# Optimization experiments

Hardware: AMD Instinct MI355X
Metric: run time of the kernel (lower is better)

Reference implementation:

```python
import jax, jax.numpy as jnp
import numpy as np

N_NODES = 10000
N_EDGES = 320000
IN_DIM = 256
HID = 64
HEADS = 4
OUT_DIM = 64
NEG_SLOPE = 0.2


def setup_inputs() -> dict:
    key = jax.random.key(0)
    ks = jax.random.split(key, 10)
    s = 0.05
    return {
        "h": jax.random.normal(ks[0], (N_NODES, IN_DIM), jnp.float32),
        "src": jax.random.randint(ks[1], (N_EDGES,), 0, N_NODES, jnp.int32),
        "dst": jax.random.randint(ks[2], (N_EDGES,), 0, N_NODES, jnp.int32),
        "W1": jax.random.normal(ks[3], (IN_DIM, HEADS * HID), jnp.float32) * s,
        "al1": jax.random.normal(ks[4], (HEADS, HID), jnp.float32) * s,
        "ar1": jax.random.normal(ks[5], (HEADS, HID), jnp.float32) * s,
        "b1": jnp.zeros((HEADS * HID,), jnp.float32),
        "W2": jax.random.normal(ks[6], (HEADS * HID, OUT_DIM), jnp.float32) * s,
        "al2": jax.random.normal(ks[7], (1, OUT_DIM), jnp.float32) * s,
        "ar2": jax.random.normal(ks[8], (1, OUT_DIM), jnp.float32) * s,
        "b2": jnp.zeros((OUT_DIM,), jnp.float32),
    }


def _gatconv(h, W, al, ar, b, src, dst, n_heads, d_out):
    """DGL-style GATConv: project, edge-softmax attention, scatter-aggregate."""
    n = h.shape[0]
    feat = (h @ W).reshape(n, n_heads, d_out)          # [N,H,D]
    el = jnp.sum(feat * al, axis=-1)                   # [N,H]
    er = jnp.sum(feat * ar, axis=-1)                   # [N,H]
    e = jax.nn.leaky_relu(el[src] + er[dst], NEG_SLOPE)  # [E,H]
    # segment softmax over incoming edges of each dst node
    m = jax.ops.segment_max(e, dst, num_segments=n)    # [N,H]
    ex = jnp.exp(e - m[dst])                           # [E,H]
    denom = jax.ops.segment_sum(ex, dst, num_segments=n)  # [N,H]
    alpha = ex / denom[dst]                            # [E,H]
    msg = feat[src] * alpha[:, :, None]                # [E,H,D]
    out = jax.ops.segment_sum(msg, dst, num_segments=n)  # [N,H,D]
    return out + b.reshape(n_heads, d_out)


def reference(h, src, dst, W1, al1, ar1, b1, W2, al2, ar2, b2):
    h1 = _gatconv(h, W1, al1, ar1, b1, src, dst, HEADS, HID)
    h1 = jax.nn.elu(h1.reshape(N_NODES, HEADS * HID))  # flatten(1) then ELU
    h2 = _gatconv(h1, W2, al2, ar2, b2, src, dst, 1, OUT_DIM)
    return jnp.squeeze(h2, axis=1)  # [N, OUT_DIM]
```

## Files before the change

kernel.cpp:

```cpp
#include <hip/hip_runtime.h>
#include <hip/hip_bf16.h>
#include <stdint.h>

#define NN 10000
#define NE 320000
#define NH 4
#define BCAP 128

#define GEMM1_MT 157
#define GEMM1_BLOCKS (GEMM1_MT * 4)
#define BUILD_BLOCKS 1250

typedef __attribute__((ext_vector_type(8))) short s16x8;
typedef __attribute__((ext_vector_type(4))) float f32x4;
typedef __attribute__((ext_vector_type(8))) unsigned short u16x8;

static __device__ __forceinline__ float b2f(unsigned short u) {
    union { unsigned int i; float f; } x; x.i = ((unsigned int)u) << 16; return x.f;
}
static __device__ __forceinline__ unsigned short f2b(float f) {
    unsigned int u = __float_as_uint(f);
    unsigned int r = (u + 0x7fffu + ((u >> 16) & 1u)) >> 16;
    return (unsigned short)r;
}

__global__ __launch_bounds__(256) void k_prep(const unsigned short* __restrict__ hraw,
                        const void* __restrict__ W1, const void* __restrict__ W2,
                        const void* al1, const void* ar1, const void* b1,
                        const void* al2, const void* ar2, const void* b2,
                        unsigned short* __restrict__ W1T, unsigned short* __restrict__ W2T,
                        unsigned short* __restrict__ canon, int* __restrict__ cnt,
                        int* __restrict__ flag) {
    __shared__ int sb[256];
    int t = threadIdx.x;
    int c = 0;
    for (int i = t; i < 2048; i += 256) {
        unsigned short u = hraw[i];
        int e = (u >> 7) & 0xFF;
        c += (e >= 97 && e <= 157) ? 1 : 0;
    }
    sb[t] = c;
    __syncthreads();
    for (int o = 128; o > 0; o >>= 1) {
        if (t < o) sb[t] += sb[t + o];
        __syncthreads();
    }
    int isbf = (sb[0] >= 1741) ? 1 : 0;

    int idx = blockIdx.x * 256 + t;
    if (idx < 65536) {
        int n = idx >> 8, k = idx & 255;
        W1T[idx] = isbf ? ((const unsigned short*)W1)[k * 256 + n]
                        : f2b(((const float*)W1)[k * 256 + n]);
    } else if (idx < 81920) {
        int j = idx - 65536;
        int n = j >> 8, k = j & 255;
        W2T[j] = isbf ? ((const unsigned short*)W2)[k * 64 + n]
                      : f2b(((const float*)W2)[k * 64 + n]);
    } else if (idx < 82880) {
        int j = idx - 81920;
        const void* srcp; int q;
        if      (j < 256) { srcp = al1; q = j; }
        else if (j < 512) { srcp = ar1; q = j - 256; }
        else if (j < 768) { srcp = b1;  q = j - 512; }
        else if (j < 832) { srcp = al2; q = j - 768; }
        else if (j < 896) { srcp = ar2; q = j - 832; }
        else              { srcp = b2;  q = j - 896; }
        canon[j] = isbf ? ((const unsigned short*)srcp)[q] : f2b(((const float*)srcp)[q]);
    } else if (idx < 92880) {
        cnt[idx - 82880] = 0;
    } else if (idx == 92880) {
        flag[0] = isbf;
    }
}

#define BSTRIDE 264
static __device__ __forceinline__ void gemm_body(short* Bs,
                        const void* __restrict__ A, const unsigned short* __restrict__ BT,
                        unsigned short* __restrict__ C,
                        float* __restrict__ el, float* __restrict__ er,
                        const unsigned short* __restrict__ al,
                        const unsigned short* __restrict__ ar,
                        int M, int N, int H, int a_isbf, int mtile, int head) {
    int t = threadIdx.x;
    int wave = t >> 6, lane = t & 63;
    int m0 = mtile * 64;
    const unsigned short* Bh = BT + (size_t)head * 64 * 256;

#pragma unroll
    for (int i = 0; i < 8; ++i) {
        int idx = t + i * 256;
        int row = idx >> 5, chunk = idx & 31;
        *(s16x8*)&Bs[row * BSTRIDE + chunk * 8] =
            *(const s16x8*)&Bh[(size_t)row * 256 + chunk * 8];
    }
    __syncthreads();

    int kq = (lane >> 4) * 8;
    const unsigned short* Ab = (const unsigned short*)A;
    const float*          Af = (const float*)A;
    int aRow = m0 + wave * 16 + (lane & 15);
    int aR = (aRow < M) ? aRow : M - 1;
    f32x4 acc[4] = {};

#pragma unroll
    for (int k0 = 0; k0 < 256; k0 += 32) {
        s16x8 afr;
        if (a_isbf) {
            afr = *(const s16x8*)&Ab[(size_t)aR * 256 + k0 + kq];
        } else {
            const float* pf = &Af[(size_t)aR * 256 + k0 + kq];
            float4 x0 = *(const float4*)pf;
            float4 x1 = *(const float4*)(pf + 4);
            afr[0] = (short)f2b(x0.x); afr[1] = (short)f2b(x0.y);
            afr[2] = (short)f2b(x0.z); afr[3] = (short)f2b(x0.w);
            afr[4] = (short)f2b(x1.x); afr[5] = (short)f2b(x1.y);
            afr[6] = (short)f2b(x1.z); afr[7] = (short)f2b(x1.w);
        }
#pragma unroll
        for (int nt = 0; nt < 4; ++nt) {
            s16x8 bfr = *(const s16x8*)&Bs[(nt * 16 + (lane & 15)) * BSTRIDE + k0 + kq];
            acc[nt] = __builtin_amdgcn_mfma_f32_16x16x32_bf16(afr, bfr, acc[nt], 0, 0, 0);
        }
    }

    float alv[4], arv[4];
#pragma unroll
    for (int nt = 0; nt < 4; ++nt) {
        int c = (lane & 15) + nt * 16;
        alv[nt] = b2f(al[head * 64 + c]);
        arv[nt] = b2f(ar[head * 64 + c]);
    }
    int col0 = head * 64 + (lane & 15);
    int r0 = m0 + wave * 16 + (lane >> 4) * 4;
    float cr[4][4];
#pragma unroll
    for (int nt = 0; nt < 4; ++nt) {
        int col = col0 + nt * 16;
#pragma unroll
        for (int i = 0; i < 4; ++i) {
            unsigned short cb = f2b(acc[nt][i]);
            cr[nt][i] = b2f(cb);
            int r = r0 + i;
            if (r < M) C[(size_t)r * N + col] = cb;
        }
    }
#pragma unroll
    for (int i = 0; i < 4; ++i) {
        float pl = 0.f, pr = 0.f;
#pragma unroll
        for (int nt = 0; nt < 4; ++nt) {
            pl += cr[nt][i] * alv[nt];
            pr += cr[nt][i] * arv[nt];
        }
#pragma unroll
        for (int o = 1; o < 16; o <<= 1) {
            pl += __shfl_xor(pl, o, 64);
            pr += __shfl_xor(pr, o, 64);
        }
        int r = r0 + i;
        if ((lane & 15) == 0 && r < M) {
            el[(size_t)r * H + head] = pl;
            er[(size_t)r * H + head] = pr;
        }
    }
}

__global__ __launch_bounds__(256) void k_g1b(const void* __restrict__ A,
                        const unsigned short* __restrict__ W1T,
                        unsigned short* __restrict__ feat1,
                        float* __restrict__ el, float* __restrict__ er,
                        const unsigned short* __restrict__ al,
                        const unsigned short* __restrict__ ar,
                        const int* __restrict__ flagp,
                        const int* __restrict__ src, const int* __restrict__ dst,
                        int* __restrict__ cnt, int* __restrict__ bucket) {
    __shared__ short Bs[64 * BSTRIDE];
    int bid = blockIdx.x;
    if (bid < GEMM1_BLOCKS) {
        int head = bid / GEMM1_MT;
        int mtile = bid - head * GEMM1_MT;
        gemm_body(Bs, A, W1T, feat1, el, er, al, ar, NN, 256, NH, flagp[0], mtile, head);
    } else {
        int i = (bid - GEMM1_BLOCKS) * 256 + threadIdx.x;
        if (i < NE) {
            int d = dst[i];
            int pos = atomicAdd(&cnt[d], 1);
            if (pos < BCAP) bucket[(d << 7) + pos] = src[i];
        }
    }
}

__global__ __launch_bounds__(256, 8) void k_e1h(const int* __restrict__ cnt,
                        const int* __restrict__ bucket,
                        const float* __restrict__ el, const float* __restrict__ er,
                        const unsigned short* __restrict__ feat,
                        const unsigned short* __restrict__ b1,
                        unsigned short* __restrict__ h1) {
    int wave = threadIdx.x >> 6, lane = threadIdx.x & 63;
    int bid = blockIdx.x;
    int head = bid / 2500;
    int node = (bid - head * 2500) * 4 + wave;
    int eg = lane >> 3, d8 = lane & 7;
    int end = cnt[node]; if (end > BCAP) end = BCAP;
    const int* bkt = bucket + ((size_t)node << 7);
    float er_d = er[(size_t)node * 4 + head];

    if (end <= 64) {
        int s = 0; float w = 0.f;
        if (lane < end) {
            s = bkt[lane];
            float x = el[(size_t)s * 4 + head] + er_d;
            x = (x >= 0.f) ? x : 0.2f * x;
            w = __expf(x);
        }
        float ls = w;
#pragma unroll
        for (int o = 1; o < 64; o <<= 1) ls += __shfl_xor(ls, o, 64);
        float a[8] = {};
        int niter = (end + 7) >> 3;
#pragma unroll 4
        for (int i = 0; i < niter; ++i) {
            int idx = 8 * i + eg;
            int   se = __shfl(s, idx, 64);
            float we = __shfl(w, idx, 64);
            u16x8 fv = *(const u16x8*)&feat[(((size_t)se * NH + head) << 6) + (d8 << 3)];
#pragma unroll
            for (int j = 0; j < 8; ++j) a[j] += we * b2f(fv[j]);
        }
#pragma unroll
        for (int j = 0; j < 8; ++j) {
            a[j] += __shfl_xor(a[j], 8, 64);
            a[j] += __shfl_xor(a[j], 16, 64);
            a[j] += __shfl_xor(a[j], 32, 64);
        }
        if (eg == 0) {
            float inv = (ls > 0.f) ? 1.f / ls : 0.f;
            u16x8 r;
#pragma unroll
            for (int j = 0; j < 8; ++j) {
                float o = a[j] * inv + b2f(b1[head * 64 + d8 * 8 + j]);
                o = (o > 0.f) ? o : (__expf(o) - 1.f);
                r[j] = f2b(o);
            }
            *(u16x8*)&h1[(((size_t)node * NH + head) << 6) + d8 * 8] = r;
        }
    } else {
        float a[8] = {};
        float ls = 0.f;
        for (int base = 0; base < end; base += 64) {
            int c = base + lane;
            int s = 0; float w = 0.f;
            if (c < end) {
                s = bkt[c];
                float x = el[(size_t)s * 4 + head] + er_d;
                x = (x >= 0.f) ? x : 0.2f * x;
                w = __expf(x);
            }
            ls += w;
            int cn = end - base; if (cn > 64) cn = 64;
            int niter = (cn + 7) >> 3;
#pragma unroll 2
            for (int i = 0; i < niter; ++i) {
                int idx = 8 * i + eg;
                int   se = __shfl(s, idx, 64);
                float we = __shfl(w, idx, 64);
                u16x8 fv = *(const u16x8*)&feat[(((size_t)se * NH + head) << 6) + (d8 << 3)];
#pragma unroll
                for (int j = 0; j < 8; ++j) a[j] += we * b2f(fv[j]);
            }
        }
#pragma unroll
        for (int o = 1; o < 64; o <<= 1) ls += __shfl_xor(ls, o, 64);
#pragma unroll
        for (int j = 0; j < 8; ++j) {
            a[j] += __shfl_xor(a[j], 8, 64);
            a[j] += __shfl_xor(a[j], 16, 64);
            a[j] += __shfl_xor(a[j], 32, 64);
        }
        if (eg == 0) {
            float inv = (ls > 0.f) ? 1.f / ls : 0.f;
            u16x8 r;
#pragma unroll
            for (int j = 0; j < 8; ++j) {
                float o = a[j] * inv + b2f(b1[head * 64 + d8 * 8 + j]);
                o = (o > 0.f) ? o : (__expf(o) - 1.f);
                r[j] = f2b(o);
            }
            *(u16x8*)&h1[(((size_t)node * NH + head) << 6) + d8 * 8] = r;
        }
    }
}

__global__ __launch_bounds__(256) void k_gemm(const void* __restrict__ A,
                                              const unsigned short* __restrict__ BT,
                                              unsigned short* __restrict__ C,
                                              float* __restrict__ el, float* __restrict__ er,
                                              const unsigned short* __restrict__ al,
                                              const unsigned short* __restrict__ ar,
                                              int M, int N, int H) {
    __shared__ short Bs[64 * BSTRIDE];
    gemm_body(Bs, A, BT, C, el, er, al, ar, M, N, H, 1, blockIdx.x, blockIdx.y);
}

__global__ __launch_bounds__(256, 4) void k_edge2(const int* __restrict__ cnt,
                        const int* __restrict__ bucket,
                        const float* __restrict__ el, const float* __restrict__ er,
                        const unsigned short* __restrict__ feat,
                        const unsigned short* __restrict__ b2,
                        void* __restrict__ out, const int* __restrict__ flagp) {
    int wave = threadIdx.x >> 6, lane = threadIdx.x & 63;
    int node = blockIdx.x * 4 + wave;
    if (node >= NN) return;
    int eg = lane >> 3, d8 = lane & 7;
    int isbf = flagp[0];
    int end = cnt[node]; if (end > BCAP) end = BCAP;
    const int* bkt = bucket + ((size_t)node << 7);
    float er_d = er[node];
    float lsum;
    float a[8] = {};

    if (end <= 64) {
        int s = 0; float wgt = 0.f;
        if (lane < end) {
            s = bkt[lane];
            float x = el[s] + er_d;
            x = (x >= 0.f) ? x : 0.2f * x;
            wgt = __expf(x);
        }
        lsum = wgt;
        int niter = (end + 7) >> 3;
#pragma unroll 4
        for (int i = 0; i < niter; ++i) {
            int idx = 8 * i + eg;
            float we = __shfl(wgt, idx, 64);
            int   se = __shfl(s, idx, 64);
            u16x8 fv = *(const u16x8*)&feat[((size_t)se << 6) + (d8 << 3)];
#pragma unroll
            for (int j = 0; j < 8; ++j) a[j] += we * b2f(fv[j]);
        }
    } else {
        lsum = 0.f;
        for (int base = 0; base < end; base += 64) {
            int c = base + lane;
            float wgt = 0.f; int s = 0;
            if (c < end) {
                s = bkt[c];
                float x = el[s] + er_d;
                x = (x >= 0.f) ? x : 0.2f * x;
                wgt = __expf(x);
            }
            lsum += wgt;
            int cn = end - base; if (cn > 64) cn = 64;
            int niter = (cn + 7) >> 3;
#pragma unroll 2
            for (int i = 0; i < niter; ++i) {
                int idx = 8 * i + eg;
                float we = __shfl(wgt, idx, 64);
                int   se = __shfl(s, idx, 64);
                u16x8 fv = *(const u16x8*)&feat[((size_t)se << 6) + (d8 << 3)];
#pragma unroll
                for (int j = 0; j < 8; ++j) a[j] += we * b2f(fv[j]);
            }
        }
    }
#pragma unroll
    for (int o = 1; o < 64; o <<= 1) lsum += __shfl_xor(lsum, o, 64);
#pragma unroll
    for (int j = 0; j < 8; ++j) {
        a[j] += __shfl_xor(a[j], 8, 64);
        a[j] += __shfl_xor(a[j], 16, 64);
        a[j] += __shfl_xor(a[j], 32, 64);
    }
    if (eg == 0) {
        float inv = (lsum > 0.f) ? 1.f / lsum : 0.f;
        float o[8];
#pragma unroll
        for (int j = 0; j < 8; ++j) o[j] = a[j] * inv + b2f(b2[d8 * 8 + j]);
        size_t ob = ((size_t)node << 6) + d8 * 8;
        if (isbf) {
            u16x8 r;
#pragma unroll
            for (int j = 0; j < 8; ++j) r[j] = f2b(o[j]);
            *(u16x8*)&((unsigned short*)out)[ob] = r;
        } else {
            float4 r0, r1;
            r0.x = o[0]; r0.y = o[1]; r0.z = o[2]; r0.w = o[3];
            r1.x = o[4]; r1.y = o[5]; r1.z = o[6]; r1.w = o[7];
            *(float4*)&((float*)out)[ob] = r0;
            *(float4*)&((float*)out)[ob + 4] = r1;
        }
    }
}

extern "C" void kernel_launch(void* const* d_in, const int* in_sizes, int n_in,
                              void* d_out, int out_size, void* d_ws, size_t ws_size,
                              hipStream_t stream) {
    const void* h   = d_in[0];
    const int*  src = (const int*)d_in[1];
    const int*  dst = (const int*)d_in[2];
    const void* W1  = d_in[3];
    const void* al1 = d_in[4];
    const void* ar1 = d_in[5];
    const void* b1  = d_in[6];
    const void* W2  = d_in[7];
    const void* al2 = d_in[8];
    const void* ar2 = d_in[9];
    const void* b2  = d_in[10];

    char* w = (char*)d_ws;
    size_t off = 0;
    auto alloc = [&](size_t bytes) -> void* {
        void* p = w + off;
        off = (off + bytes + 255) & ~(size_t)255;
        return p;
    };
    int* flag               = (int*)alloc(8);
    int* cnt                = (int*)alloc(NN * 4);
    int* bucket             = (int*)alloc((size_t)NN * BCAP * 4);
    unsigned short* canon   = (unsigned short*)alloc(960 * 2);
    unsigned short* W1T     = (unsigned short*)alloc(256 * 256 * 2);
    unsigned short* W2T     = (unsigned short*)alloc(64 * 256 * 2);
    unsigned short* feat1   = (unsigned short*)alloc((size_t)NN * 256 * 2);
    float* el1              = (float*)alloc(NN * NH * 4);
    float* er1              = (float*)alloc(NN * NH * 4);
    unsigned short* h1      = (unsigned short*)alloc((size_t)NN * 256 * 2);
    unsigned short* feat2   = (unsigned short*)alloc((size_t)NN * 64 * 2);
    float* el2              = (float*)alloc(NN * 4);
    float* er2              = (float*)alloc(NN * 4);
    (void)ws_size; (void)in_sizes; (void)n_in; (void)out_size;

    unsigned short* cal1 = canon + 0;
    unsigned short* car1 = canon + 256;
    unsigned short* cb1  = canon + 512;
    unsigned short* cal2 = canon + 768;
    unsigned short* car2 = canon + 832;
    unsigned short* cb2  = canon + 896;

    k_prep<<<363, 256, 0, stream>>>((const unsigned short*)h, W1, W2,
                                    al1, ar1, b1, al2, ar2, b2,
                                    W1T, W2T, canon, cnt, flag);
    k_g1b<<<GEMM1_BLOCKS + BUILD_BLOCKS, 256, 0, stream>>>(h, W1T, feat1, el1, er1,
                                                           cal1, car1, flag,
                                                           src, dst, cnt, bucket);
    k_e1h<<<NN, 256, 0, stream>>>(cnt, bucket, el1, er1, feat1, cb1, h1);
    k_gemm<<<dim3(GEMM1_MT, 1), 256, 0, stream>>>(h1, W2T, feat2, el2, er2,
                                                  cal2, car2, NN, 64, 1);
    k_edge2<<<(NN + 3) / 4, 256, 0, stream>>>(cnt, bucket, el2, er2, feat2, cb2, d_out, flag);
}
```

Before: 148.3 us.

## Eliminate prep kernel by fusing weight transpose and dtype detection into GEMMs

Removes the separate k_prep kernel. Each GEMM block now detects the input dtype itself, transposes and converts its weight slice straight into shared memory, and reads raw parameters with an on-the-fly conversion; the cnt array is zeroed with a memset. This drops one kernel launch and the W1T/W2T/canon round trips through global memory. In exchange every GEMM block repeats the dtype detection reduction and does strided, bank-conflicting LDS transpose writes. It also raises the k_edge2 occupancy hint from 4 to 8.

```diff
diff --git a/kernel.cpp b/kernel.cpp
--- a/kernel.cpp
+++ b/kernel.cpp
@@ -24,15 +24,7 @@
     return (unsigned short)r;
 }
 
-__global__ __launch_bounds__(256) void k_prep(const unsigned short* __restrict__ hraw,
-                        const void* __restrict__ W1, const void* __restrict__ W2,
-                        const void* al1, const void* ar1, const void* b1,
-                        const void* al2, const void* ar2, const void* b2,
-                        unsigned short* __restrict__ W1T, unsigned short* __restrict__ W2T,
-                        unsigned short* __restrict__ canon, int* __restrict__ cnt,
-                        int* __restrict__ flag) {
-    __shared__ int sb[256];
-    int t = threadIdx.x;
+static __device__ __forceinline__ int detect_isbf(const unsigned short* hraw, int t, int* sb) {
     int c = 0;
     for (int i = t; i < 2048; i += 256) {
         unsigned short u = hraw[i];
@@ -45,56 +37,48 @@
         if (t < o) sb[t] += sb[t + o];
         __syncthreads();
     }
-    int isbf = (sb[0] >= 1741) ? 1 : 0;
-
-    int idx = blockIdx.x * 256 + t;
-    if (idx < 65536) {
-        int n = idx >> 8, k = idx & 255;
-        W1T[idx] = isbf ? ((const unsigned short*)W1)[k * 256 + n]
-                        : f2b(((const float*)W1)[k * 256 + n]);
-    } else if (idx < 81920) {
-        int j = idx - 65536;
-        int n = j >> 8, k = j & 255;
-        W2T[j] = isbf ? ((const unsigned short*)W2)[k * 64 + n]
-                      : f2b(((const float*)W2)[k * 64 + n]);
-    } else if (idx < 82880) {
-        int j = idx - 81920;
-        const void* srcp; int q;
-        if      (j < 256) { srcp = al1; q = j; }
-        else if (j < 512) { srcp = ar1; q = j - 256; }
-        else if (j < 768) { srcp = b1;  q = j - 512; }
-        else if (j < 832) { srcp = al2; q = j - 768; }
-        else if (j < 896) { srcp = ar2; q = j - 832; }
-        else              { srcp = b2;  q = j - 896; }
-        canon[j] = isbf ? ((const unsigned short*)srcp)[q] : f2b(((const float*)srcp)[q]);
-    } else if (idx < 92880) {
-        cnt[idx - 82880] = 0;
-    } else if (idx == 92880) {
-        flag[0] = isbf;
-    }
+    return (sb[0] >= 1741) ? 1 : 0;
+}
+
+static __device__ __forceinline__ float ld_param(const void* p, int idx, int isbf) {
+    return isbf ? b2f(((const unsigned short*)p)[idx])
+                : b2f(f2b(((const float*)p)[idx]));
 }
 
 #define BSTRIDE 264
-static __device__ __forceinline__ void gemm_body(short* Bs,
-                        const void* __restrict__ A, const unsigned short* __restrict__ BT,
-                        unsigned short* __restrict__ C,
+static __device__ __forceinline__ void stage_bt(short* Bs, const void* W, int wcols,
+                                                int col0, int isbf, int t) {
+    int kk = t >> 3, nc = t & 7;
+#pragma unroll
+    for (int i = 0; i < 8; ++i) {
+        int k = i * 32 + kk;
+        short v[8];
+        if (isbf) {
+            s16x8 x = *(const s16x8*)((const unsigned short*)W + (size_t)k * wcols + col0 + nc * 8);
+#pragma unroll
+            for (int j = 0; j < 8; ++j) v[j] = x[j];
+        } else {
+            const float* pf = (const float*)W + (size_t)k * wcols + col0 + nc * 8;
+            float4 x0 = *(const float4*)pf;
+            float4 x1 = *(const float4*)(pf + 4);
+            v[0] = (short)f2b(x0.x); v[1] = (short)f2b(x0.y);
+            v[2] = (short)f2b(x0.z); v[3] = (short)f2b(x0.w);
+            v[4] = (short)f2b(x1.x); v[5] = (short)f2b(x1.y);
+            v[6] = (short)f2b(x1.z); v[7] = (short)f2b(x1.w);
+        }
+#pragma unroll
+        for (int j = 0; j < 8; ++j) Bs[(nc * 8 + j) * BSTRIDE + k] = v[j];
+    }
+}
+
+static __device__ __forceinline__ void gemm_core(const short* Bs,
+                        const void* __restrict__ A, unsigned short* __restrict__ C,
                         float* __restrict__ el, float* __restrict__ er,
-                        const unsigned short* __restrict__ al,
-                        const unsigned short* __restrict__ ar,
+                        const void* al_raw, const void* ar_raw, int p_isbf,
                         int M, int N, int H, int a_isbf, int mtile, int head) {
     int t = threadIdx.x;
     int wave = t >> 6, lane = t & 63;
     int m0 = mtile * 64;
-    const unsigned short* Bh = BT + (size_t)head * 64 * 256;
-
-#pragma unroll
-    for (int i = 0; i < 8; ++i) {
-        int idx = t + i * 256;
-        int row = idx >> 5, chunk = idx & 31;
-        *(s16x8*)&Bs[row * BSTRIDE + chunk * 8] =
-            *(const s16x8*)&Bh[(size_t)row * 256 + chunk * 8];
-    }
-    __syncthreads();
 
     int kq = (lane >> 4) * 8;
     const unsigned short* Ab = (const unsigned short*)A;
@@ -128,8 +112,8 @@
 #pragma unroll
     for (int nt = 0; nt < 4; ++nt) {
         int c = (lane & 15) + nt * 16;
-        alv[nt] = b2f(al[head * 64 + c]);
-        arv[nt] = b2f(ar[head * 64 + c]);
+        alv[nt] = ld_param(al_raw, head * 64 + c, p_isbf);
+        arv[nt] = ld_param(ar_raw, head * 64 + c, p_isbf);
     }
     int col0 = head * 64 + (lane & 15);
     int r0 = m0 + wave * 16 + (lane >> 4) * 4;
@@ -167,22 +151,27 @@
 }
 
 __global__ __launch_bounds__(256) void k_g1b(const void* __restrict__ A,
-                        const unsigned short* __restrict__ W1T,
+                        const void* __restrict__ W1,
                         unsigned short* __restrict__ feat1,
                         float* __restrict__ el, float* __restrict__ er,
-                        const unsigned short* __restrict__ al,
-                        const unsigned short* __restrict__ ar,
-                        const int* __restrict__ flagp,
+                        const void* __restrict__ al1, const void* __restrict__ ar1,
                         const int* __restrict__ src, const int* __restrict__ dst,
-                        int* __restrict__ cnt, int* __restrict__ bucket) {
+                        int* __restrict__ cnt, int* __restrict__ bucket,
+                        int* __restrict__ flag) {
     __shared__ short Bs[64 * BSTRIDE];
+    __shared__ int sb[256];
     int bid = blockIdx.x;
+    int t = threadIdx.x;
     if (bid < GEMM1_BLOCKS) {
+        int isbf = detect_isbf((const unsigned short*)A, t, sb);
+        if (bid == 0 && t == 0) flag[0] = isbf;
         int head = bid / GEMM1_MT;
         int mtile = bid - head * GEMM1_MT;
-        gemm_body(Bs, A, W1T, feat1, el, er, al, ar, NN, 256, NH, flagp[0], mtile, head);
+        stage_bt(Bs, W1, 256, head * 64, isbf, t);
+        __syncthreads();
+        gemm_core(Bs, A, feat1, el, er, al1, ar1, isbf, NN, 256, NH, isbf, mtile, head);
     } else {
-        int i = (bid - GEMM1_BLOCKS) * 256 + threadIdx.x;
+        int i = (bid - GEMM1_BLOCKS) * 256 + t;
         if (i < NE) {
             int d = dst[i];
             int pos = atomicAdd(&cnt[d], 1);
@@ -195,13 +184,15 @@
                         const int* __restrict__ bucket,
                         const float* __restrict__ el, const float* __restrict__ er,
                         const unsigned short* __restrict__ feat,
-                        const unsigned short* __restrict__ b1,
+                        const void* __restrict__ b1,
+                        const int* __restrict__ flagp,
                         unsigned short* __restrict__ h1) {
     int wave = threadIdx.x >> 6, lane = threadIdx.x & 63;
     int bid = blockIdx.x;
     int head = bid / 2500;
     int node = (bid - head * 2500) * 4 + wave;
     int eg = lane >> 3, d8 = lane & 7;
+    int isbf = flagp[0];
     int end = cnt[node]; if (end > BCAP) end = BCAP;
     const int* bkt = bucket + ((size_t)node << 7);
     float er_d = er[(size_t)node * 4 + head];
@@ -239,7 +230,7 @@
             u16x8 r;
 #pragma unroll
             for (int j = 0; j < 8; ++j) {
-                float o = a[j] * inv + b2f(b1[head * 64 + d8 * 8 + j]);
+                float o = a[j] * inv + ld_param(b1, head * 64 + d8 * 8 + j, isbf);
                 o = (o > 0.f) ? o : (__expf(o) - 1.f);
                 r[j] = f2b(o);
             }
@@ -283,7 +274,7 @@
             u16x8 r;
 #pragma unroll
             for (int j = 0; j < 8; ++j) {
-                float o = a[j] * inv + b2f(b1[head * 64 + d8 * 8 + j]);
+                float o = a[j] * inv + ld_param(b1, head * 64 + d8 * 8 + j, isbf);
                 o = (o > 0.f) ? o : (__expf(o) - 1.f);
                 r[j] = f2b(o);
             }
@@ -293,21 +284,25 @@
 }
 
 __global__ __launch_bounds__(256) void k_gemm(const void* __restrict__ A,
-                                              const unsigned short* __restrict__ BT,
+                                              const void* __restrict__ W2,
                                               unsigned short* __restrict__ C,
                                               float* __restrict__ el, float* __restrict__ er,
-                                              const unsigned short* __restrict__ al,
-                                              const unsigned short* __restrict__ ar,
+                                              const void* __restrict__ al2,
+                                              const void* __restrict__ ar2,
+                                              const int* __restrict__ flagp,
                                               int M, int N, int H) {
     __shared__ short Bs[64 * BSTRIDE];
-    gemm_body(Bs, A, BT, C, el, er, al, ar, M, N, H, 1, blockIdx.x, blockIdx.y);
-}
-
-__global__ __launch_bounds__(256, 4) void k_edge2(const int* __restrict__ cnt,
+    int isbf = flagp[0];
+    stage_bt(Bs, W2, 64, 0, isbf, threadIdx.x);
+    __syncthreads();
+    gemm_core(Bs, A, C, el, er, al2, ar2, isbf, M, N, H, 1, blockIdx.x, 0);
+}
+
+__global__ __launch_bounds__(256, 8) void k_edge2(const int* __restrict__ cnt,
                         const int* __restrict__ bucket,
                         const float* __restrict__ el, const float* __restrict__ er,
                         const unsigned short* __restrict__ feat,
-                        const unsigned short* __restrict__ b2,
+                        const void* __restrict__ b2,
                         void* __restrict__ out, const int* __restrict__ flagp) {
     int wave = threadIdx.x >> 6, lane = threadIdx.x & 63;
     int node = blockIdx.x * 4 + wave;
@@ -376,7 +371,7 @@
         float inv = (lsum > 0.f) ? 1.f / lsum : 0.f;
         float o[8];
 #pragma unroll
-        for (int j = 0; j < 8; ++j) o[j] = a[j] * inv + b2f(b2[d8 * 8 + j]);
+        for (int j = 0; j < 8; ++j) o[j] = a[j] * inv + ld_param(b2, d8 * 8 + j, isbf);
         size_t ob = ((size_t)node << 6) + d8 * 8;
         if (isbf) {
             u16x8 r;
@@ -418,9 +413,6 @@
     int* flag               = (int*)alloc(8);
     int* cnt                = (int*)alloc(NN * 4);
     int* bucket             = (int*)alloc((size_t)NN * BCAP * 4);
-    unsigned short* canon   = (unsigned short*)alloc(960 * 2);
-    unsigned short* W1T     = (unsigned short*)alloc(256 * 256 * 2);
-    unsigned short* W2T     = (unsigned short*)alloc(64 * 256 * 2);
     unsigned short* feat1   = (unsigned short*)alloc((size_t)NN * 256 * 2);
     float* el1              = (float*)alloc(NN * NH * 4);
     float* er1              = (float*)alloc(NN * NH * 4);
@@ -430,21 +422,12 @@
     float* er2              = (float*)alloc(NN * 4);
     (void)ws_size; (void)in_sizes; (void)n_in; (void)out_size;
 
-    unsigned short* cal1 = canon + 0;
-    unsigned short* car1 = canon + 256;
-    unsigned short* cb1  = canon + 512;
-    unsigned short* cal2 = canon + 768;
-    unsigned short* car2 = canon + 832;
-    unsigned short* cb2  = canon + 896;
-
-    k_prep<<<363, 256, 0, stream>>>((const unsigned short*)h, W1, W2,
-                                    al1, ar1, b1, al2, ar2, b2,
-                                    W1T, W2T, canon, cnt, flag);
-    k_g1b<<<GEMM1_BLOCKS + BUILD_BLOCKS, 256, 0, stream>>>(h, W1T, feat1, el1, er1,
-                                                           cal1, car1, flag,
-                                                           src, dst, cnt, bucket);
-    k_e1h<<<NN, 256, 0, stream>>>(cnt, bucket, el1, er1, feat1, cb1, h1);
-    k_gemm<<<dim3(GEMM1_MT, 1), 256, 0, stream>>>(h1, W2T, feat2, el2, er2,
-                                                  cal2, car2, NN, 64, 1);
-    k_edge2<<<(NN + 3) / 4, 256, 0, stream>>>(cnt, bucket, el2, er2, feat2, cb2, d_out, flag);
-}
+    hipMemsetAsync(cnt, 0, NN * sizeof(int), stream);
+    k_g1b<<<GEMM1_BLOCKS + BUILD_BLOCKS, 256, 0, stream>>>(h, W1, feat1, el1, er1,
+                                                           al1, ar1, src, dst,
+                                                           cnt, bucket, flag);
+    k_e1h<<<NN, 256, 0, stream>>>(cnt, bucket, el1, er1, feat1, b1, flag, h1);
+    k_gemm<<<dim3(GEMM1_MT, 1), 256, 0, stream>>>(h1, W2, feat2, el2, er2,
+                                                  al2, ar2, flag, NN, 64, 1);
+    k_edge2<<<(NN + 3) / 4, 256, 0, stream>>>(cnt, bucket, el2, er2, feat2, b2, d_out, flag);
+}
```

After: 162.9 us. 1.1x slower.
